# Kernel optimization log

Measured on AMD Instinct MI355X. Metric: run time of the kernel, lower is better.

Reference implementation:

```python
import jax, jax.numpy as jnp
import numpy as np

LOG2PI = float(np.log(2.0 * np.pi))

INPUT_DIM, HIDDEN_DIM, OUTPUT_DIM, HORIZON = 128, 2048, 128, 1024


def setup_inputs() -> dict:
    key = jax.random.key(0)
    ks = jax.random.split(key, 10)
    s = 0.02
    return {
        "s0": jax.random.normal(ks[0], (HORIZON, INPUT_DIM), jnp.float32),
        "eps": jax.random.normal(ks[1], (HORIZON, OUTPUT_DIM), jnp.float32),
        "W_ih": jax.random.normal(ks[2], (4 * HIDDEN_DIM, INPUT_DIM), jnp.float32) * s,
        "W_hh": jax.random.normal(ks[3], (4 * HIDDEN_DIM, HIDDEN_DIM), jnp.float32) * s,
        "b_ih": jax.random.normal(ks[4], (4 * HIDDEN_DIM,), jnp.float32) * s,
        "b_hh": jax.random.normal(ks[5], (4 * HIDDEN_DIM,), jnp.float32) * s,
        "W_mu": jax.random.normal(ks[6], (OUTPUT_DIM, HIDDEN_DIM), jnp.float32) * s,
        "b_mu": jax.random.normal(ks[7], (OUTPUT_DIM,), jnp.float32) * s,
        "W_lv": jax.random.normal(ks[8], (OUTPUT_DIM, HIDDEN_DIM), jnp.float32) * s,
        "b_lv": jax.random.normal(ks[9], (OUTPUT_DIM,), jnp.float32) * s,
        "H": HORIZON,
    }


def reference(s0, eps, W_ih, W_hh, b_ih, b_hh, W_mu, b_mu, W_lv, b_lv, H):
    hd = W_hh.shape[1]

    def step(carry, inp):
        h, c = carry  # [hidden], [hidden]
        x, e = inp    # [input_dim], [output_dim]
        gates = W_ih @ x + b_ih + W_hh @ h + b_hh  # [4*hidden]
        i, f, g, o = jnp.split(gates, 4)
        i, f, o = jax.nn.sigmoid(i), jax.nn.sigmoid(f), jax.nn.sigmoid(o)
        g = jnp.tanh(g)
        c = f * c + i * g
        h = o * jnp.tanh(c)
        mu = W_mu @ h + b_mu
        logvar = W_lv @ h + b_lv
        std = jnp.exp(0.5 * logvar)
        # Normal.sample() is detached from the graph in torch
        x_samp = jax.lax.stop_gradient(mu + std * e)
        lp = -0.5 * jnp.square((x_samp - mu) / std) - jnp.log(std) - 0.5 * LOG2PI
        return (h, c), (x_samp, lp, h)

    h0 = jnp.zeros((hd,), s0.dtype)
    c0 = jnp.zeros((hd,), s0.dtype)
    _, (xs, lps, hs) = jax.lax.scan(step, (h0, c0), (s0[:H], eps[:H]))
    return xs, lps, hs  # [H, out], [H, out], [H, hidden]
```

## Files before the change

### kernel.cpp

```cpp
#include <hip/hip_runtime.h>
#include <math.h>

#define TSTEPS 1024
#define HID    2048
#define IN_D   128
#define OUT_D  128
#define NWG    256
#define NTHR   512
#define NPAIRS (HID / 2)

#define LOG2PI_F 1.8378770664093453f

typedef unsigned long long u64;
typedef unsigned int       u32;

static __device__ __forceinline__ u32 bf16_rne(float f) {
    u32 u = __float_as_uint(f);
    return (u + 0x7FFFu + ((u >> 16) & 1u)) >> 16;
}
static __device__ __forceinline__ float bf16_lo(u32 payload) {
    return __uint_as_float(payload << 16);
}
static __device__ __forceinline__ float bf16_hi(u32 payload) {
    return __uint_as_float(payload & 0xFFFF0000u);
}
static __device__ __forceinline__ float fast_sig(float x) {
    return __builtin_amdgcn_rcpf(1.0f + __expf(-x));
}
static __device__ __forceinline__ float fast_tanh(float x) {
    return 1.0f - 2.0f * __builtin_amdgcn_rcpf(1.0f + __expf(2.0f * x));
}

__global__ __launch_bounds__(NTHR)
void lstm_persist(const float* __restrict__ s0,
                  const float* __restrict__ Wih,
                  const float* __restrict__ Whh,
                  const float* __restrict__ bih,
                  const float* __restrict__ bhh,
                  float* __restrict__ hs_out,
                  u64* __restrict__ pairs)
{
    __shared__ __align__(16) float4 ldsH[2][HID / 4];
    __shared__ __align__(16) float  gsum[32];

    const int tid   = threadIdx.x;
    const int wg    = blockIdx.x;
    const int hbase = wg * 8;
    const int rg    = tid >> 6;
    const int lane  = tid & 63;

    float w[4][32];
    float wih2[4][2];
    float breg[4];
#pragma unroll
    for (int m = 0; m < 4; ++m) {
        const int li = rg * 4 + m;
        const int grow = (li >> 3) * HID + hbase + (li & 7);
        const float4* src = (const float4*)(Whh + (size_t)grow * HID + lane * 32);
#pragma unroll
        for (int q = 0; q < 8; ++q) {
            float4 v = src[q];
            w[m][4*q+0] = v.x; w[m][4*q+1] = v.y;
            w[m][4*q+2] = v.z; w[m][4*q+3] = v.w;
        }
        wih2[m][0] = Wih[(size_t)grow * IN_D + 2 * lane];
        wih2[m][1] = Wih[(size_t)grow * IN_D + 2 * lane + 1];
        breg[m]    = bih[grow] + bhh[grow];
    }

    float2 c2 = make_float2(0.f, 0.f);

    for (int t = 0; t < TSTEPS; ++t) {
        const int slot = (t - 1) & 1;

        const float2 xv = *(const float2*)(s0 + (size_t)t * IN_D + 2 * lane);
        float acc[4];
#pragma unroll
        for (int m = 0; m < 4; ++m)
            acc[m] = wih2[m][0] * xv.x + wih2[m][1] * xv.y;

        if (t > 0 && rg == 0) {
            const u32 want = (u32)t;
            const u64* base = pairs + (size_t)slot * NPAIRS;
            u64 v[16];
            for (;;) {
                int ok = 1;
#pragma unroll
                for (int j = 0; j < 16; ++j) {
                    v[j] = __hip_atomic_load(base + 64 * j + lane,
                                             __ATOMIC_RELAXED, __HIP_MEMORY_SCOPE_AGENT);
                    ok &= ((u32)(v[j] >> 32) == want);
                }
                if (__all(ok)) break;
                __builtin_amdgcn_s_sleep(1);
            }
#pragma unroll
            for (int j = 0; j < 16; ++j) {
                const int idx  = 64 * j + lane;
                const int cch  = idx >> 1;
                const int half = idx & 1;
                const int p    = cch ^ ((cch >> 3) & 7);
                float* dst = (float*)&ldsH[slot][p] + 2 * half;
                *(float2*)dst = make_float2(bf16_lo((u32)v[j]), bf16_hi((u32)v[j]));
            }
        }
        __syncthreads();

        if (t > 0) {
#pragma unroll
            for (int j = 0; j < 8; ++j) {
                const int p = (8 * lane + j) ^ (lane & 7);
                float4 hv = ldsH[slot][p];
#pragma unroll
                for (int m = 0; m < 4; ++m) {
                    acc[m] += hv.x * w[m][4*j+0];
                    acc[m] += hv.y * w[m][4*j+1];
                    acc[m] += hv.z * w[m][4*j+2];
                    acc[m] += hv.w * w[m][4*j+3];
                }
            }
        }

#pragma unroll
        for (int m = 0; m < 4; ++m) {
            acc[m] += __shfl_xor(acc[m], 1);
            acc[m] += __shfl_xor(acc[m], 2);
            acc[m] += __shfl_xor(acc[m], 4);
            acc[m] += __shfl_xor(acc[m], 8);
            acc[m] += __shfl_xor(acc[m], 16);
            acc[m] += __shfl_xor(acc[m], 32);
        }
        if (lane == 0) {
            *(float4*)&gsum[rg * 4] = make_float4(acc[0] + breg[0], acc[1] + breg[1],
                                                  acc[2] + breg[2], acc[3] + breg[3]);
        }
        __syncthreads();

        if (tid < 4) {
            const int j0 = 2 * tid, j1 = 2 * tid + 1;
            const float i0 = fast_sig (gsum[j0]),      i1 = fast_sig (gsum[j1]);
            const float f0 = fast_sig (gsum[8  + j0]), f1 = fast_sig (gsum[8  + j1]);
            const float g0 = fast_tanh(gsum[16 + j0]), g1 = fast_tanh(gsum[16 + j1]);
            const float o0 = fast_sig (gsum[24 + j0]), o1 = fast_sig (gsum[24 + j1]);
            c2.x = f0 * c2.x + i0 * g0;
            c2.y = f1 * c2.y + i1 * g1;
            const float h0 = o0 * fast_tanh(c2.x);
            const float h1 = o1 * fast_tanh(c2.y);
            const u64 pkt = (u64)(bf16_rne(h0) | (bf16_rne(h1) << 16))
                          | ((u64)(u32)(t + 1) << 32);
            __hip_atomic_store(&pairs[(size_t)(t & 1) * NPAIRS + wg * 4 + tid], pkt,
                               __ATOMIC_RELAXED, __HIP_MEMORY_SCOPE_AGENT);
            *(float2*)&hs_out[(size_t)t * HID + hbase + j0] = make_float2(h0, h1);
        }
    }
}

__global__ __launch_bounds__(256)
void out_head(const float* __restrict__ eps,
              const float* __restrict__ Wmu,
              const float* __restrict__ bmu,
              const float* __restrict__ Wlv,
              const float* __restrict__ blv,
              const float* __restrict__ hs,
              float* __restrict__ xs,
              float* __restrict__ lp)
{
    __shared__ __align__(16) float hlds[4][HID];
    __shared__ __align__(16) float exch[4][256];

    const int tid = threadIdx.x;
    const int t0  = blockIdx.x * 4;

    {
        const float4* src = (const float4*)(hs + (size_t)t0 * HID);
        float4* dst = (float4*)&hlds[0][0];
#pragma unroll
        for (int i = 0; i < 8; ++i)
            dst[tid + i * 256] = src[tid + i * 256];
    }
    __syncthreads();

    const int  jrow  = tid & 127;
    const bool is_lv = tid >= 128;
    const float* Wrow = (is_lv ? Wlv : Wmu) + (size_t)jrow * HID;
    const float  bias = is_lv ? blv[jrow] : bmu[jrow];

    float acc[4] = {0.f, 0.f, 0.f, 0.f};
    const float4* w4 = (const float4*)Wrow;
#pragma unroll 4
    for (int kq = 0; kq < HID / 4; ++kq) {
        float4 wv = w4[kq];
#pragma unroll
        for (int tt = 0; tt < 4; ++tt) {
            float4 hv = ((const float4*)&hlds[tt][0])[kq];
            acc[tt] += wv.x * hv.x + wv.y * hv.y + wv.z * hv.z + wv.w * hv.w;
        }
    }
#pragma unroll
    for (int tt = 0; tt < 4; ++tt) exch[tt][tid] = acc[tt] + bias;
    __syncthreads();

#pragma unroll
    for (int r = 0; r < 2; ++r) {
        const int item = tid + r * 256;
        const int tt = item >> 7;
        const int jj = item & 127;
        const int t  = t0 + tt;
        const float mu = exch[tt][jj];
        const float lv = exch[tt][128 + jj];
        const float e  = eps[(size_t)t * OUT_D + jj];
        const float sd = expf(0.5f * lv);
        const float x  = mu + sd * e;
        const float d  = (x - mu) / sd;
        const float l  = -0.5f * d * d - 0.5f * lv - 0.5f * LOG2PI_F;
        xs[(size_t)t * OUT_D + jj] = x;
        lp[(size_t)t * OUT_D + jj] = l;
    }
}

extern "C" void kernel_launch(void* const* d_in, const int* in_sizes, int n_in,
                              void* d_out, int out_size, void* d_ws, size_t ws_size,
                              hipStream_t stream)
{
    (void)in_sizes; (void)n_in; (void)out_size; (void)ws_size;

    const float* s0  = (const float*)d_in[0];
    const float* eps = (const float*)d_in[1];
    const float* Wih = (const float*)d_in[2];
    const float* Whh = (const float*)d_in[3];
    const float* bih = (const float*)d_in[4];
    const float* bhh = (const float*)d_in[5];
    const float* Wmu = (const float*)d_in[6];
    const float* bmu = (const float*)d_in[7];
    const float* Wlv = (const float*)d_in[8];
    const float* blv = (const float*)d_in[9];

    float* out = (float*)d_out;
    float* xs = out;
    float* lp = out + TSTEPS * OUT_D;
    float* hs = out + 2 * TSTEPS * OUT_D;

    u64* pairs = (u64*)d_ws;

    (void)hipMemsetAsync(d_ws, 0, 2 * NPAIRS * sizeof(u64), stream);

    hipLaunchKernelGGL(lstm_persist, dim3(NWG), dim3(NTHR), 0, stream,
                       s0, Wih, Whh, bih, bhh, hs, pairs);

    hipLaunchKernelGGL(out_head, dim3(TSTEPS / 4), dim3(256), 0, stream,
                       eps, Wmu, bmu, Wlv, blv, hs, xs, lp);
}
```

Baseline: 2.971 ms.

## Assign one hidden cell per wavefront and store raw packed pairs in LDS

Reassigns W_hh rows so each wavefront owns all four gates of a single hidden cell, letting lane 0 compute the LSTM cell update directly from its reduced accumulators instead of going through a shared gate-sum buffer and a separate 4-thread stage. The polling of the global h-exchange is split across two wavefronts with half the loads each, and the packed bf16 pairs are written raw to LDS, with unpacking deferred to the matvec read. This shortens the per-step serial critical path between the barrier and the global publish. The cost is extra bit ops in the inner loop and half-used 128-bit LDS reads.

```diff
diff --git a/kernel.cpp b/kernel.cpp
--- a/kernel.cpp
+++ b/kernel.cpp
@@ -17,12 +17,6 @@
 static __device__ __forceinline__ u32 bf16_rne(float f) {
     u32 u = __float_as_uint(f);
     return (u + 0x7FFFu + ((u >> 16) & 1u)) >> 16;
-}
-static __device__ __forceinline__ float bf16_lo(u32 payload) {
-    return __uint_as_float(payload << 16);
-}
-static __device__ __forceinline__ float bf16_hi(u32 payload) {
-    return __uint_as_float(payload & 0xFFFF0000u);
 }
 static __device__ __forceinline__ float fast_sig(float x) {
     return __builtin_amdgcn_rcpf(1.0f + __expf(-x));
@@ -40,22 +34,22 @@
                   float* __restrict__ hs_out,
                   u64* __restrict__ pairs)
 {
-    __shared__ __align__(16) float4 ldsH[2][HID / 4];
-    __shared__ __align__(16) float  gsum[32];
+    __shared__ __align__(16) u64 ldsP[2][NPAIRS];
+    __shared__ __align__(16) u64 cellbuf[8];
 
     const int tid   = threadIdx.x;
     const int wg    = blockIdx.x;
     const int hbase = wg * 8;
     const int rg    = tid >> 6;
     const int lane  = tid & 63;
+    const int cell  = hbase + rg;
 
     float w[4][32];
     float wih2[4][2];
     float breg[4];
 #pragma unroll
     for (int m = 0; m < 4; ++m) {
-        const int li = rg * 4 + m;
-        const int grow = (li >> 3) * HID + hbase + (li & 7);
+        const int grow = m * HID + cell;
         const float4* src = (const float4*)(Whh + (size_t)grow * HID + lane * 32);
 #pragma unroll
         for (int q = 0; q < 8; ++q) {
@@ -68,7 +62,7 @@
         breg[m]    = bih[grow] + bhh[grow];
     }
 
-    float2 c2 = make_float2(0.f, 0.f);
+    float c = 0.0f;
 
     for (int t = 0; t < TSTEPS; ++t) {
         const int slot = (t - 1) & 1;
@@ -79,14 +73,14 @@
         for (int m = 0; m < 4; ++m)
             acc[m] = wih2[m][0] * xv.x + wih2[m][1] * xv.y;
 
-        if (t > 0 && rg == 0) {
+        if (t > 0 && rg < 2) {
             const u32 want = (u32)t;
-            const u64* base = pairs + (size_t)slot * NPAIRS;
-            u64 v[16];
+            const u64* base = pairs + (size_t)slot * NPAIRS + rg * 512;
+            u64 v[8];
             for (;;) {
                 int ok = 1;
 #pragma unroll
-                for (int j = 0; j < 16; ++j) {
+                for (int j = 0; j < 8; ++j) {
                     v[j] = __hip_atomic_load(base + 64 * j + lane,
                                              __ATOMIC_RELAXED, __HIP_MEMORY_SCOPE_AGENT);
                     ok &= ((u32)(v[j] >> 32) == want);
@@ -95,13 +89,11 @@
                 __builtin_amdgcn_s_sleep(1);
             }
 #pragma unroll
-            for (int j = 0; j < 16; ++j) {
-                const int idx  = 64 * j + lane;
+            for (int j = 0; j < 8; ++j) {
+                const int idx  = rg * 512 + 64 * j + lane;
                 const int cch  = idx >> 1;
-                const int half = idx & 1;
                 const int p    = cch ^ ((cch >> 3) & 7);
-                float* dst = (float*)&ldsH[slot][p] + 2 * half;
-                *(float2*)dst = make_float2(bf16_lo((u32)v[j]), bf16_hi((u32)v[j]));
+                ldsP[slot][2 * p + (idx & 1)] = v[j];
             }
         }
         __syncthreads();
@@ -110,13 +102,17 @@
 #pragma unroll
             for (int j = 0; j < 8; ++j) {
                 const int p = (8 * lane + j) ^ (lane & 7);
-                float4 hv = ldsH[slot][p];
+                const uint4 q = *(const uint4*)&ldsP[slot][2 * p];
+                const float h0 = __uint_as_float(q.x << 16);
+                const float h1 = __uint_as_float(q.x & 0xFFFF0000u);
+                const float h2 = __uint_as_float(q.z << 16);
+                const float h3 = __uint_as_float(q.z & 0xFFFF0000u);
 #pragma unroll
                 for (int m = 0; m < 4; ++m) {
-                    acc[m] += hv.x * w[m][4*j+0];
-                    acc[m] += hv.y * w[m][4*j+1];
-                    acc[m] += hv.z * w[m][4*j+2];
-                    acc[m] += hv.w * w[m][4*j+3];
+                    acc[m] += h0 * w[m][4*j+0];
+                    acc[m] += h1 * w[m][4*j+1];
+                    acc[m] += h2 * w[m][4*j+2];
+                    acc[m] += h3 * w[m][4*j+3];
                 }
             }
         }
@@ -130,27 +126,27 @@
             acc[m] += __shfl_xor(acc[m], 16);
             acc[m] += __shfl_xor(acc[m], 32);
         }
+
         if (lane == 0) {
-            *(float4*)&gsum[rg * 4] = make_float4(acc[0] + breg[0], acc[1] + breg[1],
-                                                  acc[2] + breg[2], acc[3] + breg[3]);
+            const float ig = fast_sig (acc[0] + breg[0]);
+            const float fg = fast_sig (acc[1] + breg[1]);
+            const float gg = fast_tanh(acc[2] + breg[2]);
+            const float og = fast_sig (acc[3] + breg[3]);
+            c = fg * c + ig * gg;
+            const float h = og * fast_tanh(c);
+            cellbuf[rg] = ((u64)bf16_rne(h) << 32) | (u64)__float_as_uint(h);
         }
         __syncthreads();
 
         if (tid < 4) {
-            const int j0 = 2 * tid, j1 = 2 * tid + 1;
-            const float i0 = fast_sig (gsum[j0]),      i1 = fast_sig (gsum[j1]);
-            const float f0 = fast_sig (gsum[8  + j0]), f1 = fast_sig (gsum[8  + j1]);
-            const float g0 = fast_tanh(gsum[16 + j0]), g1 = fast_tanh(gsum[16 + j1]);
-            const float o0 = fast_sig (gsum[24 + j0]), o1 = fast_sig (gsum[24 + j1]);
-            c2.x = f0 * c2.x + i0 * g0;
-            c2.y = f1 * c2.y + i1 * g1;
-            const float h0 = o0 * fast_tanh(c2.x);
-            const float h1 = o1 * fast_tanh(c2.y);
-            const u64 pkt = (u64)(bf16_rne(h0) | (bf16_rne(h1) << 16))
-                          | ((u64)(u32)(t + 1) << 32);
-            __hip_atomic_store(&pairs[(size_t)(t & 1) * NPAIRS + wg * 4 + tid], pkt,
+            const u64 cb0 = cellbuf[2 * tid];
+            const u64 cb1 = cellbuf[2 * tid + 1];
+            const u64 pair = (((u64)(u32)(t + 1)) << 32)
+                           | (u64)(((u32)(cb0 >> 32)) | (((u32)(cb1 >> 32)) << 16));
+            __hip_atomic_store(&pairs[(size_t)(t & 1) * NPAIRS + wg * 4 + tid], pair,
                                __ATOMIC_RELAXED, __HIP_MEMORY_SCOPE_AGENT);
-            *(float2*)&hs_out[(size_t)t * HID + hbase + j0] = make_float2(h0, h1);
+            *(float2*)&hs_out[(size_t)t * HID + hbase + 2 * tid] =
+                make_float2(__uint_as_float((u32)cb0), __uint_as_float((u32)cb1));
         }
     }
 }
```

Result: no change. 2.985 ms (+0.5%).
